# Optimization experiments

Measured on AMD Instinct MI355X. Metric: run time of the kernel, lower is better.

The kernel has to match this reference:

```python
import jax, jax.numpy as jnp
import numpy as np

IMAGE_SIZE = 224          # config.image_size
RP_Q = 10 / 100.0         # config.rp_percentage, 'point' threshold mode
EPS = 1e-8                # normalize_minmax eps
CLIP = 1e-6               # arccos clamp margin


def minmax_global(x):
    """normalize_minmax over the whole tensor (as applied to the raw series)."""
    lo, hi = x.min(), x.max()
    rng = hi - lo
    return jnp.where(rng < EPS, jnp.zeros_like(x), (x - lo) / (rng + EPS))


def minmax_per_matrix(x):
    """normalize_minmax applied independently per (b, d) LxL matrix."""
    lo = x.min(axis=(-2, -1), keepdims=True)
    hi = x.max(axis=(-2, -1), keepdims=True)
    rng = hi - lo
    return jnp.where(rng < EPS, jnp.zeros_like(x), (x - lo) / (rng + EPS))


def setup_inputs() -> dict:
    key = jax.random.key(0)
    x = jax.random.normal(key, (4, 1024, 8), dtype=jnp.float32)  # [B, L, D]
    return {"x": x}


def reference(x):
    B, L, D = x.shape

    # ---- Gramian Angular Field (summation), vectorized over (b, d) ----
    x_norm = minmax_global(x) * 2.0 - 1.0                       # [B, L, D]
    theta = jnp.arccos(jnp.clip(x_norm, -1.0 + CLIP, 1.0 - CLIP))
    th = jnp.transpose(theta, (0, 2, 1))                        # [B, D, L]
    gaf = jnp.cos(th[:, :, :, None] + th[:, :, None, :])        # [B, D, L, L]
    gaf = minmax_per_matrix(gaf)

    # ---- Recurrence plot ('point' quantile threshold), vectorized ----
    s = jnp.transpose(x, (0, 2, 1))                             # [B, D, L]
    dist = jnp.abs(s[:, :, :, None] - s[:, :, None, :])         # [B, D, L, L]
    thr = jnp.quantile(dist.reshape(B, D, L * L), RP_Q, axis=-1)
    rp = (dist <= thr[:, :, None, None]).astype(x.dtype)        # [B, D, L, L]

    # ---- Bilinear resize to (image_size, image_size), align_corners=False ----
    out = jnp.concatenate([gaf, rp], axis=1)                    # [B, 2D, L, L]
    out = jax.image.resize(out, (B, 2 * D, IMAGE_SIZE, IMAGE_SIZE),
                           method="bilinear", antialias=False)
    return out
```

## Files before the change

kernel.cpp:

```cpp
#include <hip/hip_runtime.h>
#include <cfloat>
#include <math.h>

#define B_ 4
#define L_ 1024
#define D_ 8
#define OUT_ 224
#define NPIX (B_ * 2 * D_ * OUT_ * OUT_)
#define NT4  (NPIX / 4)
#define PI_F 3.14159265358979323846f

__device__ __forceinline__ float clipnorm(float v, float lo, float inv2, int degen) {
    float xn = degen ? -1.0f : ((v - lo) * inv2 - 1.0f);
    return fminf(fmaxf(xn, -1.0f + 1e-6f), 1.0f - 1e-6f);
}

__device__ __forceinline__ unsigned fkey(float f) {
    unsigned u = __float_as_uint(f);
    return (u & 0x80000000u) ? ~u : (u | 0x80000000u);
}
__device__ __forceinline__ float unfkey(unsigned k) {
    unsigned u = (k & 0x80000000u) ? (k ^ 0x80000000u) : ~k;
    return __uint_as_float(u);
}

__global__ __launch_bounds__(1024) void k_stats(const float* __restrict__ x,
                                                float* __restrict__ ws) {
    __shared__ float t[L_];
    __shared__ float csort[L_];
    __shared__ float ssort[L_];
    __shared__ float w[L_];
    __shared__ unsigned cnt_buf[2];
    __shared__ unsigned umin_a, umax_a, umin_b, umax_b, succ_bits;

    const int tid  = threadIdx.x;
    const int lane = tid & 63;
    const int blk  = blockIdx.x;
    const int b = blk >> 3, d = blk & 7;

    if (tid == 0) {
        umin_a = 0xFFFFFFFFu; umax_a = 0u;
        umin_b = 0xFFFFFFFFu; umax_b = 0u;
        succ_bits = 0xFFFFFFFFu;
        cnt_buf[0] = 0u; cnt_buf[1] = 0u;
    }
    __syncthreads();

    {
        const float4* x4 = (const float4*)x;
        float lo = FLT_MAX, hi = -FLT_MAX;
        for (int i = tid; i < (B_ * L_ * D_) / 4; i += 1024) {
            float4 q = x4[i];
            lo = fminf(fminf(fminf(lo, q.x), q.y), fminf(q.z, q.w));
            hi = fmaxf(fmaxf(fmaxf(hi, q.x), q.y), fmaxf(q.z, q.w));
        }
#pragma unroll
        for (int off = 32; off; off >>= 1) {
            lo = fminf(lo, __shfl_down(lo, off));
            hi = fmaxf(hi, __shfl_down(hi, off));
        }
        if (lane == 0) { atomicMin(&umin_a, fkey(lo)); atomicMax(&umax_a, fkey(hi)); }
    }
    __syncthreads();
    const float glo = unfkey(umin_a), ghi = unfkey(umax_a);
    if (blk == 0 && tid == 0) { ws[0] = glo; ws[1] = ghi; }
    const float rng  = ghi - glo;
    const int degen  = rng < 1e-8f;
    const float inv2 = 2.0f / (rng + 1e-8f);

    float v = x[(b * L_ + tid) * D_ + d];
    for (int k = 2; k <= L_; k <<= 1) {
        bool up = ((tid & k) == 0);
        for (int j = k >> 1; j > 0; j >>= 1) {
            bool lower = ((tid & j) == 0);
            float other;
            if (j >= 64) {
                __syncthreads();
                t[tid] = v;
                __syncthreads();
                other = t[tid ^ j];
            } else {
                other = __shfl_xor(v, j);
            }
            float mn = fminf(v, other), mx = fmaxf(v, other);
            v = (lower == up) ? mn : mx;
        }
    }
    __syncthreads();
    t[tid] = v;

    {
        float c = clipnorm(v, glo, inv2, degen);
        csort[tid] = c;
        ssort[tid] = sqrtf(fmaxf(0.0f, 1.0f - c * c));
        w[tid]     = acosf(c);
    }
    __syncthreads();

    {
        float wi = w[tid];
        int jstar = -1;
        if (wi + w[0] >= PI_F) {
            int a = 0, bh = L_ - 1;
            while (a < bh) { int m = (a + bh + 1) >> 1; if (wi + w[m] >= PI_F) a = m; else bh = m - 1; }
            jstar = a;
        }
        float ci = csort[tid], si = ssort[tid];
        float mn = FLT_MAX, mx = -FLT_MAX;
        int cands[4] = {0, L_ - 1, jstar, jstar + 1};
#pragma unroll
        for (int q = 0; q < 4; q++) {
            int j = cands[q];
            if (j >= 0 && j < L_) {
                float g = ci * csort[j] - si * ssort[j];
                mn = fminf(mn, g); mx = fmaxf(mx, g);
            }
        }
#pragma unroll
        for (int off = 32; off; off >>= 1) {
            mn = fminf(mn, __shfl_down(mn, off));
            mx = fmaxf(mx, __shfl_down(mx, off));
        }
        if (lane == 0) { atomicMin(&umin_b, fkey(mn)); atomicMax(&umax_b, fkey(mx)); }
        __syncthreads();
        if (tid == 0) {
            ws[2 + blk * 3 + 0] = unfkey(umin_b);
            ws[2 + blk * 3 + 1] = unfkey(umax_b);
        }
    }

    int pass = 0;
    auto block_sum = [&](unsigned cnt) -> unsigned {
#pragma unroll
        for (int off = 32; off; off >>= 1) cnt += __shfl_down(cnt, off);
        if (lane == 0) atomicAdd(&cnt_buf[pass & 1], cnt);
        __syncthreads();
        unsigned tot = cnt_buf[pass & 1];
        if (tid == 0) cnt_buf[(pass + 1) & 1] = 0u;
        __syncthreads();
        pass++;
        return tot;
    };

    const float ti = v;
    int jloA; { int a2 = 0, b2 = tid;
        while (a2 < b2) { int m2 = (a2 + b2) >> 1; if (ti - t[m2] <= 0.0f) b2 = m2; else a2 = m2 + 1; }
        jloA = a2; }
    int jhiA; { int a2 = tid, b2 = L_ - 1;
        while (a2 < b2) { int m2 = (a2 + b2 + 1) >> 1; if (t[m2] - ti <= 0.0f) a2 = m2; else b2 = m2 - 1; }
        jhiA = a2; }
    int jloB = 0, jhiB = L_ - 1;

    const unsigned k1 = 104858u, k2 = 104859u;
    const float dmax = t[L_ - 1] - t[0];

    unsigned tot0 = block_sum((unsigned)(jhiA - jloA + 1));
    float v1;
    unsigned cnt_at_v1;
    if (tot0 >= k1) {
        v1 = 0.0f; cnt_at_v1 = tot0;
        jloB = jloA; jhiB = jhiA;
    } else {
        unsigned lob = 0u, hib = __float_as_uint(dmax);
        cnt_at_v1 = (unsigned)(L_ * L_);
        while (hib - lob > 1u) {
            unsigned midb = lob + ((hib - lob) >> 1);
            float vm = __uint_as_float(midb);
            int jloM; { int a2 = jloB, b2 = jloA;
                while (a2 < b2) { int m2 = (a2 + b2) >> 1; if (ti - t[m2] <= vm) b2 = m2; else a2 = m2 + 1; }
                jloM = a2; }
            int jhiM; { int a2 = jhiA, b2 = jhiB;
                while (a2 < b2) { int m2 = (a2 + b2 + 1) >> 1; if (t[m2] - ti <= vm) a2 = m2; else b2 = m2 - 1; }
                jhiM = a2; }
            unsigned tot = block_sum((unsigned)(jhiM - jloM + 1));
            if (tot >= k1) { hib = midb; jloB = jloM; jhiB = jhiM; cnt_at_v1 = tot; }
            else           { lob = midb; jloA = jloM; jhiA = jhiM; }
        }
        v1 = __uint_as_float(hib);
    }

    float thr;
    if (cnt_at_v1 >= k2) {
        thr = v1;
    } else {
        float s = FLT_MAX;
        if (jloB > 0)      s = fminf(s, ti - t[jloB - 1]);
        if (jhiB < L_ - 1) s = fminf(s, t[jhiB + 1] - ti);
#pragma unroll
        for (int off = 32; off; off >>= 1) s = fminf(s, __shfl_down(s, off));
        if (lane == 0) atomicMin(&succ_bits, __float_as_uint(s));
        __syncthreads();
        float v2 = __uint_as_float(succ_bits);
        thr = v1 + (v2 - v1) * 0.5f;
    }
    if (tid == 0) ws[2 + blk * 3 + 2] = thr;
}

__global__ __launch_bounds__(256) void k_out(const float* __restrict__ x,
                                             const float* __restrict__ ws,
                                             float4* __restrict__ out4) {
    int tix = blockIdx.x * 256 + threadIdx.x;
    int pix0 = tix << 2;
    int ox0 = pix0 % OUT_;
    int t1  = pix0 / OUT_;
    int oy  = t1 % OUT_;
    int t2  = t1 / OUT_;
    int c   = t2 & 15;
    int b   = t2 >> 4;

    const float scale = (float)L_ / (float)OUT_;
    float fy = (oy + 0.5f) * scale - 0.5f;
    int y0 = (int)fy; float wy = fy - (float)y0;

    int d = c & 7;
    const float* xb = x + b * (L_ * D_) + d;
    float r0 = xb[y0 * D_], r1 = xb[(y0 + 1) * D_];

    float res[4];
    if (c < 8) {
        float lo = ws[0], hi = ws[1];
        float rngg = hi - lo;
        int degen  = rngg < 1e-8f;
        float inv2 = 2.0f / (rngg + 1e-8f);
        float mn = ws[2 + (b * 8 + d) * 3 + 0];
        float mx = ws[2 + (b * 8 + d) * 3 + 1];
        float grng = mx - mn;
        int gdeg   = grng < 1e-8f;
        float ginv = 1.0f / (grng + 1e-8f);
        float cr0 = clipnorm(r0, lo, inv2, degen), cr1 = clipnorm(r1, lo, inv2, degen);
        float sr0 = sqrtf(fmaxf(0.0f, 1.0f - cr0 * cr0)), sr1 = sqrtf(fmaxf(0.0f, 1.0f - cr1 * cr1));
#pragma unroll
        for (int p = 0; p < 4; p++) {
            float fx = (ox0 + p + 0.5f) * scale - 0.5f;
            int x0 = (int)fx; float wx = fx - (float)x0;
            float q0 = xb[x0 * D_], q1 = xb[(x0 + 1) * D_];
            float cq0 = clipnorm(q0, lo, inv2, degen), cq1 = clipnorm(q1, lo, inv2, degen);
            float sq0 = sqrtf(fmaxf(0.0f, 1.0f - cq0 * cq0)), sq1 = sqrtf(fmaxf(0.0f, 1.0f - cq1 * cq1));
            float v00 = gdeg ? 0.0f : (cr0 * cq0 - sr0 * sq0 - mn) * ginv;
            float v01 = gdeg ? 0.0f : (cr0 * cq1 - sr0 * sq1 - mn) * ginv;
            float v10 = gdeg ? 0.0f : (cr1 * cq0 - sr1 * sq0 - mn) * ginv;
            float v11 = gdeg ? 0.0f : (cr1 * cq1 - sr1 * sq1 - mn) * ginv;
            float top = v00 + wx * (v01 - v00);
            float bot = v10 + wx * (v11 - v10);
            res[p] = top + wy * (bot - top);
        }
    } else {
        float thr = ws[2 + (b * 8 + d) * 3 + 2];
#pragma unroll
        for (int p = 0; p < 4; p++) {
            float fx = (ox0 + p + 0.5f) * scale - 0.5f;
            int x0 = (int)fx; float wx = fx - (float)x0;
            float q0 = xb[x0 * D_], q1 = xb[(x0 + 1) * D_];
            float v00 = (fabsf(r0 - q0) <= thr) ? 1.0f : 0.0f;
            float v01 = (fabsf(r0 - q1) <= thr) ? 1.0f : 0.0f;
            float v10 = (fabsf(r1 - q0) <= thr) ? 1.0f : 0.0f;
            float v11 = (fabsf(r1 - q1) <= thr) ? 1.0f : 0.0f;
            float top = v00 + wx * (v01 - v00);
            float bot = v10 + wx * (v11 - v10);
            res[p] = top + wy * (bot - top);
        }
    }
    out4[tix] = make_float4(res[0], res[1], res[2], res[3]);
}

extern "C" void kernel_launch(void* const* d_in, const int* in_sizes, int n_in,
                              void* d_out, int out_size, void* d_ws, size_t ws_size,
                              hipStream_t stream) {
    const float* x = (const float*)d_in[0];
    float* ws = (float*)d_ws;

    k_stats<<<B_ * D_, 1024, 0, stream>>>(x, ws);
    k_out<<<NT4 / 256, 256, 0, stream>>>(x, ws, (float4*)d_out);
}
```

Baseline: 111.7 us.

## Precompute separable GAF tables and use 8-way quantile bisection

The quantile threshold search now tests seven candidate values per round instead of one. This cuts the number of block-wide reductions and barriers in the bisection by about a factor of three. k_stats also writes per-(b,d) tables: bilinearly interpolated cos and sin values for the GAF, and gathered sample pairs for the RP. k_out reads these from LDS instead of gathering x and recomputing sqrt per pixel. The GAF interpolation is factored into a product of interpolated cos and sin terms, which is not exactly equal to bilinear interpolation of the product, so results may drift.

```diff
diff --git a/kernel.cpp b/kernel.cpp
--- a/kernel.cpp
+++ b/kernel.cpp
@@ -9,12 +9,13 @@
 #define NPIX (B_ * 2 * D_ * OUT_ * OUT_)
 #define NT4  (NPIX / 4)
 #define PI_F 3.14159265358979323846f
+#define TBL 128
+#define TSTR 896
 
 __device__ __forceinline__ float clipnorm(float v, float lo, float inv2, int degen) {
     float xn = degen ? -1.0f : ((v - lo) * inv2 - 1.0f);
     return fminf(fmaxf(xn, -1.0f + 1e-6f), 1.0f - 1e-6f);
 }
-
 __device__ __forceinline__ unsigned fkey(float f) {
     unsigned u = __float_as_uint(f);
     return (u & 0x80000000u) ? ~u : (u | 0x80000000u);
@@ -27,10 +28,8 @@
 __global__ __launch_bounds__(1024) void k_stats(const float* __restrict__ x,
                                                 float* __restrict__ ws) {
     __shared__ float t[L_];
-    __shared__ float csort[L_];
-    __shared__ float ssort[L_];
-    __shared__ float w[L_];
-    __shared__ unsigned cnt_buf[2];
+    __shared__ float csort[L_], ssort[L_], w[L_];
+    __shared__ unsigned cbuf[2][8];
     __shared__ unsigned umin_a, umax_a, umin_b, umax_b, succ_bits;
 
     const int tid  = threadIdx.x;
@@ -42,8 +41,8 @@
         umin_a = 0xFFFFFFFFu; umax_a = 0u;
         umin_b = 0xFFFFFFFFu; umax_b = 0u;
         succ_bits = 0xFFFFFFFFu;
-        cnt_buf[0] = 0u; cnt_buf[1] = 0u;
-    }
+    }
+    if (tid < 16) ((unsigned*)cbuf)[tid] = 0u;
     __syncthreads();
 
     {
@@ -67,6 +66,25 @@
     const float rng  = ghi - glo;
     const int degen  = rng < 1e-8f;
     const float inv2 = 2.0f / (rng + 1e-8f);
+
+    if (tid < 2 * OUT_) {
+        const float scale = (float)L_ / (float)OUT_;
+        int o = tid & 255; if (tid >= OUT_) o = tid - OUT_;
+        float fx = (o + 0.5f) * scale - 0.5f;
+        int x0 = (int)fx; float wx = fx - (float)x0;
+        float q0 = x[(b * L_ + x0) * D_ + d];
+        float q1 = x[(b * L_ + x0 + 1) * D_ + d];
+        float* base = ws + TBL + blk * TSTR;
+        if (tid < OUT_) {
+            float c0 = clipnorm(q0, glo, inv2, degen), c1 = clipnorm(q1, glo, inv2, degen);
+            float s0 = sqrtf(fmaxf(0.0f, 1.0f - c0 * c0)), s1 = sqrtf(fmaxf(0.0f, 1.0f - c1 * c1));
+            base[o]        = c0 + wx * (c1 - c0);
+            base[OUT_ + o] = s0 + wx * (s1 - s0);
+        } else {
+            base[448 + o] = q0;
+            base[672 + o] = q1;
+        }
+    }
 
     float v = x[(b * L_ + tid) * D_ + d];
     for (int k = 2; k <= L_; k <<= 1) {
@@ -129,63 +147,131 @@
         }
     }
 
+    const float ti = v;
     int pass = 0;
-    auto block_sum = [&](unsigned cnt) -> unsigned {
-#pragma unroll
-        for (int off = 32; off; off >>= 1) cnt += __shfl_down(cnt, off);
-        if (lane == 0) atomicAdd(&cnt_buf[pass & 1], cnt);
+
+    int jlo0; { int a2 = 0, b2 = tid;
+        while (a2 < b2) { int m2 = (a2 + b2) >> 1; if (ti - t[m2] <= 0.0f) b2 = m2; else a2 = m2 + 1; }
+        jlo0 = a2; }
+    int jhi0; { int a2 = tid, b2 = L_ - 1;
+        while (a2 < b2) { int m2 = (a2 + b2 + 1) >> 1; if (t[m2] - ti <= 0.0f) a2 = m2; else b2 = m2 - 1; }
+        jhi0 = a2; }
+
+    unsigned tot0;
+    {
+        unsigned c0 = (unsigned)(jhi0 - jlo0 + 1);
+#pragma unroll
+        for (int off = 32; off; off >>= 1) c0 += __shfl_down(c0, off);
+        if (lane == 0) atomicAdd(&cbuf[0][1], c0);
         __syncthreads();
-        unsigned tot = cnt_buf[pass & 1];
-        if (tid == 0) cnt_buf[(pass + 1) & 1] = 0u;
+        tot0 = cbuf[0][1];
+        if (tid < 8) cbuf[1][tid] = 0u;
         __syncthreads();
-        pass++;
-        return tot;
-    };
-
-    const float ti = v;
-    int jloA; { int a2 = 0, b2 = tid;
-        while (a2 < b2) { int m2 = (a2 + b2) >> 1; if (ti - t[m2] <= 0.0f) b2 = m2; else a2 = m2 + 1; }
-        jloA = a2; }
-    int jhiA; { int a2 = tid, b2 = L_ - 1;
-        while (a2 < b2) { int m2 = (a2 + b2 + 1) >> 1; if (t[m2] - ti <= 0.0f) a2 = m2; else b2 = m2 - 1; }
-        jhiA = a2; }
-    int jloB = 0, jhiB = L_ - 1;
+        pass = 1;
+    }
 
     const unsigned k1 = 104858u, k2 = 104859u;
     const float dmax = t[L_ - 1] - t[0];
 
-    unsigned tot0 = block_sum((unsigned)(jhiA - jloA + 1));
-    float v1;
-    unsigned cnt_at_v1;
+    float v1; unsigned cntV1; int jloV1, jhiV1;
     if (tot0 >= k1) {
-        v1 = 0.0f; cnt_at_v1 = tot0;
-        jloB = jloA; jhiB = jhiA;
+        v1 = 0.0f; cntV1 = tot0; jloV1 = jlo0; jhiV1 = jhi0;
     } else {
-        unsigned lob = 0u, hib = __float_as_uint(dmax);
-        cnt_at_v1 = (unsigned)(L_ * L_);
-        while (hib - lob > 1u) {
-            unsigned midb = lob + ((hib - lob) >> 1);
-            float vm = __uint_as_float(midb);
-            int jloM; { int a2 = jloB, b2 = jloA;
-                while (a2 < b2) { int m2 = (a2 + b2) >> 1; if (ti - t[m2] <= vm) b2 = m2; else a2 = m2 + 1; }
-                jloM = a2; }
-            int jhiM; { int a2 = jhiA, b2 = jhiB;
-                while (a2 < b2) { int m2 = (a2 + b2 + 1) >> 1; if (t[m2] - ti <= vm) a2 = m2; else b2 = m2 - 1; }
-                jhiM = a2; }
-            unsigned tot = block_sum((unsigned)(jhiM - jloM + 1));
-            if (tot >= k1) { hib = midb; jloB = jloM; jhiB = jhiM; cnt_at_v1 = tot; }
-            else           { lob = midb; jloA = jloM; jhiA = jhiM; }
-        }
-        v1 = __uint_as_float(hib);
+        unsigned vlo = 0u, vhi = __float_as_uint(dmax);
+        unsigned cntHi = (unsigned)(L_ * L_);
+        int jloLo = jlo0, jhiLo = jhi0;
+        int jloHi = 0,    jhiHi = L_ - 1;
+        unsigned cntLo = tot0; (void)cntLo;
+
+        while (vhi - vlo > 1u) {
+            unsigned width = vhi - vlo;
+            int ne = (width - 1u < 7u) ? (int)(width - 1u) : 7;
+            unsigned vb[8]; float vf[8];
+#pragma unroll
+            for (int e = 1; e <= 7; e++) {
+                unsigned off = (unsigned)(((unsigned long long)width * (unsigned)e) / (unsigned)(ne + 1));
+                vb[e] = vlo + off;
+                vf[e] = __uint_as_float(vb[e]);
+            }
+            int aL[8], bL[8], aH[8], bH[8];
+#pragma unroll
+            for (int e = 1; e <= 7; e++) { aL[e] = jloHi; bL[e] = jloLo; aH[e] = jhiLo; bH[e] = jhiHi; }
+            bool any = true;
+            while (any) {
+                any = false;
+                float tvL[8], tvH[8];
+                bool acL[8], acH[8];
+#pragma unroll
+                for (int e = 1; e <= 7; e++) {
+                    acL[e] = (e <= ne) && (aL[e] < bL[e]);
+                    if (acL[e]) tvL[e] = t[(aL[e] + bL[e]) >> 1];
+                    acH[e] = (e <= ne) && (aH[e] < bH[e]);
+                    if (acH[e]) tvH[e] = t[(aH[e] + bH[e] + 1) >> 1];
+                }
+#pragma unroll
+                for (int e = 1; e <= 7; e++) {
+                    if (acL[e]) {
+                        int m = (aL[e] + bL[e]) >> 1;
+                        if (ti - tvL[e] <= vf[e]) bL[e] = m; else aL[e] = m + 1;
+                        any = true;
+                    }
+                    if (acH[e]) {
+                        int m = (aH[e] + bH[e] + 1) >> 1;
+                        if (tvH[e] - ti <= vf[e]) aH[e] = m; else bH[e] = m - 1;
+                        any = true;
+                    }
+                }
+            }
+            int pb = pass & 1;
+#pragma unroll
+            for (int e = 1; e <= 7; e++) {
+                if (e <= ne) {
+                    unsigned c = (unsigned)(aH[e] - aL[e] + 1);
+#pragma unroll
+                    for (int off = 32; off; off >>= 1) c += __shfl_down(c, off);
+                    if (lane == 0) atomicAdd(&cbuf[pb][e], c);
+                }
+            }
+            __syncthreads();
+            unsigned tot[8];
+#pragma unroll
+            for (int e = 1; e <= 7; e++) tot[e] = cbuf[pb][e];
+            if (tid < 8) cbuf[(pass + 1) & 1][tid] = 0u;
+            __syncthreads();
+            pass++;
+
+            int estar = 0;
+#pragma unroll
+            for (int e = 7; e >= 1; e--) if (e <= ne && tot[e] >= k1) estar = e;
+
+            if (estar == 0) {
+#pragma unroll
+                for (int e = 1; e <= 7; e++) if (e == ne) {
+                    vlo = vb[e]; jloLo = aL[e]; jhiLo = aH[e];
+                }
+            } else {
+#pragma unroll
+                for (int e = 1; e <= 7; e++) if (e == estar) {
+                    vhi = vb[e]; cntHi = tot[e]; jloHi = aL[e]; jhiHi = aH[e];
+                }
+                if (estar > 1) {
+#pragma unroll
+                    for (int e = 1; e <= 7; e++) if (e == estar - 1) {
+                        vlo = vb[e]; jloLo = aL[e]; jhiLo = aH[e];
+                    }
+                }
+            }
+        }
+        v1 = __uint_as_float(vhi); cntV1 = cntHi; jloV1 = jloHi; jhiV1 = jhiHi;
     }
 
     float thr;
-    if (cnt_at_v1 >= k2) {
+    if (cntV1 >= k2) {
         thr = v1;
     } else {
         float s = FLT_MAX;
-        if (jloB > 0)      s = fminf(s, ti - t[jloB - 1]);
-        if (jhiB < L_ - 1) s = fminf(s, t[jhiB + 1] - ti);
+        if (jloV1 > 0)      s = fminf(s, ti - t[jloV1 - 1]);
+        if (jhiV1 < L_ - 1) s = fminf(s, t[jhiV1 + 1] - ti);
 #pragma unroll
         for (int off = 32; off; off >>= 1) s = fminf(s, __shfl_down(s, off));
         if (lane == 0) atomicMin(&succ_bits, __float_as_uint(s));
@@ -196,61 +282,57 @@
     if (tid == 0) ws[2 + blk * 3 + 2] = thr;
 }
 
-__global__ __launch_bounds__(256) void k_out(const float* __restrict__ x,
-                                             const float* __restrict__ ws,
+__global__ __launch_bounds__(256) void k_out(const float* __restrict__ ws,
                                              float4* __restrict__ out4) {
-    int tix = blockIdx.x * 256 + threadIdx.x;
+    __shared__ float lds[448];
+    __shared__ float sc[3];
+
+    const int tid = threadIdx.x;
+    int plane = blockIdx.x / 49;
+    int c = plane & 15, b = plane >> 4, d = c & 7;
+
+    const float* tb = ws + TBL + (b * 8 + d) * TSTR + ((c < 8) ? 0 : 448);
+    for (int i = tid; i < 448; i += 256) lds[i] = tb[i];
+    if (tid == 0) {
+        if (c < 8) {
+            float mn = ws[2 + (b * 8 + d) * 3 + 0];
+            float mx = ws[2 + (b * 8 + d) * 3 + 1];
+            float g = mx - mn;
+            sc[0] = mn;
+            sc[1] = (g < 1e-8f) ? 0.0f : 1.0f / (g + 1e-8f);
+            sc[2] = (g < 1e-8f) ? 1.0f : 0.0f;
+        } else {
+            sc[0] = ws[2 + (b * 8 + d) * 3 + 2];
+        }
+    }
+    __syncthreads();
+
+    int tix = blockIdx.x * 256 + tid;
     int pix0 = tix << 2;
     int ox0 = pix0 % OUT_;
-    int t1  = pix0 / OUT_;
-    int oy  = t1 % OUT_;
-    int t2  = t1 / OUT_;
-    int c   = t2 & 15;
-    int b   = t2 >> 4;
-
-    const float scale = (float)L_ / (float)OUT_;
-    float fy = (oy + 0.5f) * scale - 0.5f;
-    int y0 = (int)fy; float wy = fy - (float)y0;
-
-    int d = c & 7;
-    const float* xb = x + b * (L_ * D_) + d;
-    float r0 = xb[y0 * D_], r1 = xb[(y0 + 1) * D_];
+    int oy  = (pix0 / OUT_) % OUT_;
 
     float res[4];
     if (c < 8) {
-        float lo = ws[0], hi = ws[1];
-        float rngg = hi - lo;
-        int degen  = rngg < 1e-8f;
-        float inv2 = 2.0f / (rngg + 1e-8f);
-        float mn = ws[2 + (b * 8 + d) * 3 + 0];
-        float mx = ws[2 + (b * 8 + d) * 3 + 1];
-        float grng = mx - mn;
-        int gdeg   = grng < 1e-8f;
-        float ginv = 1.0f / (grng + 1e-8f);
-        float cr0 = clipnorm(r0, lo, inv2, degen), cr1 = clipnorm(r1, lo, inv2, degen);
-        float sr0 = sqrtf(fmaxf(0.0f, 1.0f - cr0 * cr0)), sr1 = sqrtf(fmaxf(0.0f, 1.0f - cr1 * cr1));
+        float mn = sc[0], ginv = sc[1];
+        bool gdeg = sc[2] != 0.0f;
+        float Cr = lds[oy], Sr = lds[OUT_ + oy];
+#pragma unroll
+        for (int p = 0; p < 4; p++) {
+            float g = Cr * lds[ox0 + p] - Sr * lds[OUT_ + ox0 + p];
+            res[p] = gdeg ? 0.0f : (g - mn) * ginv;
+        }
+    } else {
+        float thr = sc[0];
+        const float scale = (float)L_ / (float)OUT_;
+        float fy = (oy + 0.5f) * scale - 0.5f;
+        int y0 = (int)fy; float wy = fy - (float)y0;
+        float r0 = lds[oy], r1 = lds[OUT_ + oy];
 #pragma unroll
         for (int p = 0; p < 4; p++) {
             float fx = (ox0 + p + 0.5f) * scale - 0.5f;
             int x0 = (int)fx; float wx = fx - (float)x0;
-            float q0 = xb[x0 * D_], q1 = xb[(x0 + 1) * D_];
-            float cq0 = clipnorm(q0, lo, inv2, degen), cq1 = clipnorm(q1, lo, inv2, degen);
-            float sq0 = sqrtf(fmaxf(0.0f, 1.0f - cq0 * cq0)), sq1 = sqrtf(fmaxf(0.0f, 1.0f - cq1 * cq1));
-            float v00 = gdeg ? 0.0f : (cr0 * cq0 - sr0 * sq0 - mn) * ginv;
-            float v01 = gdeg ? 0.0f : (cr0 * cq1 - sr0 * sq1 - mn) * ginv;
-            float v10 = gdeg ? 0.0f : (cr1 * cq0 - sr1 * sq0 - mn) * ginv;
-            float v11 = gdeg ? 0.0f : (cr1 * cq1 - sr1 * sq1 - mn) * ginv;
-            float top = v00 + wx * (v01 - v00);
-            float bot = v10 + wx * (v11 - v10);
-            res[p] = top + wy * (bot - top);
-        }
-    } else {
-        float thr = ws[2 + (b * 8 + d) * 3 + 2];
-#pragma unroll
-        for (int p = 0; p < 4; p++) {
-            float fx = (ox0 + p + 0.5f) * scale - 0.5f;
-            int x0 = (int)fx; float wx = fx - (float)x0;
-            float q0 = xb[x0 * D_], q1 = xb[(x0 + 1) * D_];
+            float q0 = lds[ox0 + p], q1 = lds[OUT_ + ox0 + p];
             float v00 = (fabsf(r0 - q0) <= thr) ? 1.0f : 0.0f;
             float v01 = (fabsf(r0 - q1) <= thr) ? 1.0f : 0.0f;
             float v10 = (fabsf(r1 - q0) <= thr) ? 1.0f : 0.0f;
@@ -270,5 +352,5 @@
     float* ws = (float*)d_ws;
 
     k_stats<<<B_ * D_, 1024, 0, stream>>>(x, ws);
-    k_out<<<NT4 / 256, 256, 0, stream>>>(x, ws, (float4*)d_out);
-}
+    k_out<<<NT4 / 256, 256, 0, stream>>>(ws, (float4*)d_out);
+}
```

New measurement: 182.4 us. 1.63x slower.
